# Optimization experiments

Hardware: AMD Instinct MI355X
Metric: run time of the kernel (lower is better)

Reference implementation:

```python
import jax, jax.numpy as jnp
import numpy as np

BN_EPS = 1e-5
LRELU_SLOPE = 0.2


def setup_inputs() -> dict:
    key = jax.random.key(0)
    ks = jax.random.split(key, 5)
    B, C1, M, C2, N, C_out = 8, 256, 4096, 128, 16384, 256
    feature = jax.random.normal(ks[0], (B, C1, M), dtype=jnp.float32)
    encoder_feature = jax.random.normal(ks[1], (B, C2, N), dtype=jnp.float32)
    interp_index = jax.random.randint(ks[2], (B, N, 1), 0, M, dtype=jnp.int64)
    # ConvTranspose1d(384, 256, 1) weight has shape [in, out, 1] -> store as [in, out]
    W = jax.random.normal(ks[3], (C1 + C2, C_out), dtype=jnp.float32) * 0.05
    b = jax.random.normal(ks[4], (C_out,), dtype=jnp.float32) * 0.05
    gamma = jnp.ones((C_out,), dtype=jnp.float32)
    beta = jnp.zeros((C_out,), dtype=jnp.float32)
    return {"feature": feature, "encoder_feature": encoder_feature,
            "interp_index": interp_index, "W": W, "b": b,
            "gamma": gamma, "beta": beta}


def reference(feature, encoder_feature, interp_index, W, b, gamma, beta):
    # feature: [B, C1, M], encoder_feature: [B, C2, N], interp_index: [B, N, 1]
    idx = interp_index[..., 0]                                  # [B, N]
    # index_points on feature.permute(0,2,1) then permute back == gather along last dim
    interp_feature = jnp.take_along_axis(feature, idx[:, None, :], axis=2)  # [B, C1, N]
    x = jnp.concatenate([encoder_feature, interp_feature], axis=1)          # [B, C1+C2, N]
    # ConvTranspose1d(kernel=1): y[b,o,n] = sum_i x[b,i,n] * W[i,o] + b[o]
    y = jnp.einsum('bin,io->bon', x, W) + b[None, :, None]      # [B, C_out, N]
    # BatchNorm1d (training mode: batch stats over (B, N), biased variance)
    mean = jnp.mean(y, axis=(0, 2), keepdims=True)
    var = jnp.mean(jnp.square(y - mean), axis=(0, 2), keepdims=True)
    y = (y - mean) * jax.lax.rsqrt(var + BN_EPS)
    y = y * gamma[None, :, None] + beta[None, :, None]
    # LeakyReLU(0.2)
    return jnp.where(y > 0, y, LRELU_SLOPE * y)
```

## Files before the change

### kernel.cpp

```cpp
#include <hip/hip_runtime.h>
#include <hip/hip_bf16.h>

#define C1    256
#define C2    128
#define COUT  256
#define MM    4096
#define NN    16384
#define BB    8
#define BN_EPS 1e-5f
#define SLOPE 0.2f

typedef float  f32x4  __attribute__((ext_vector_type(4)));
typedef __bf16 bf16x8 __attribute__((ext_vector_type(8)));
typedef unsigned short u16x8 __attribute__((ext_vector_type(8)));

#define GLOBAL_AS __attribute__((address_space(1)))
#define LDS_AS    __attribute__((address_space(3)))

static __device__ __forceinline__ unsigned short f2bf(float f) {
    unsigned int u = __builtin_bit_cast(unsigned int, f);
    unsigned int r = (u + 0x7FFFu + ((u >> 16) & 1u)) >> 16;
    return (unsigned short)r;
}

static __device__ __forceinline__ bf16x8 ld_frag(const unsigned short* p) {
    union { u16x8 s; bf16x8 b; } cvt;
    cvt.s = *reinterpret_cast<const u16x8*>(p);
    return cvt.b;
}

__global__ __launch_bounds__(256, 4) void k1_zt(const float* __restrict__ feature,
                                                const float* __restrict__ W,
                                                float* __restrict__ Zt) {
    const int mt = blockIdx.x;
    const int ot = blockIdx.y;
    const int b  = blockIdx.z;
    const int mb = mt * 64, ob = ot * 64;
    const int tid = threadIdx.x;

    __shared__ unsigned short sA[64 * 136];
    __shared__ unsigned short sB[64 * 136];

    const int wid = tid >> 6, lane = tid & 63;
    const int r = lane & 15, g = lane >> 4;
    const int wm = (wid >> 1) * 32, wo = (wid & 1) * 32;

    f32x4 acc[2][2];
#pragma unroll
    for (int i = 0; i < 2; i++)
#pragma unroll
        for (int j = 0; j < 2; j++) acc[i][j] = (f32x4){0.f, 0.f, 0.f, 0.f};

    for (int kp = 0; kp < 2; kp++) {
        const int k0 = kp * 128;
        for (int p = tid; p < 64 * 16; p += 256) {
            int m = p & 63, k = (p >> 6) << 3;
            u16x8 u;
#pragma unroll
            for (int j = 0; j < 8; j++)
                u[j] = f2bf(feature[(size_t)(b * C1 + k0 + k + j) * MM + mb + m]);
            *reinterpret_cast<u16x8*>(&sA[m * 136 + k]) = u;
        }
        for (int p = tid; p < 64 * 16; p += 256) {
            int o = p & 63, k = (p >> 6) << 3;
            u16x8 u;
#pragma unroll
            for (int j = 0; j < 8; j++)
                u[j] = f2bf(W[(C2 + k0 + k + j) * COUT + ob + o]);
            *reinterpret_cast<u16x8*>(&sB[o * 136 + k]) = u;
        }
        __syncthreads();

#pragma unroll
        for (int ks = 0; ks < 4; ks++) {
            const int kb = ks * 32 + g * 8;
            bf16x8 a0 = ld_frag(&sA[(wm +  0 + r) * 136 + kb]);
            bf16x8 a1 = ld_frag(&sA[(wm + 16 + r) * 136 + kb]);
            bf16x8 b0 = ld_frag(&sB[(wo +  0 + r) * 136 + kb]);
            bf16x8 b1 = ld_frag(&sB[(wo + 16 + r) * 136 + kb]);
            acc[0][0] = __builtin_amdgcn_mfma_f32_16x16x32_bf16(a0, b0, acc[0][0], 0, 0, 0);
            acc[0][1] = __builtin_amdgcn_mfma_f32_16x16x32_bf16(a0, b1, acc[0][1], 0, 0, 0);
            acc[1][0] = __builtin_amdgcn_mfma_f32_16x16x32_bf16(a1, b0, acc[1][0], 0, 0, 0);
            acc[1][1] = __builtin_amdgcn_mfma_f32_16x16x32_bf16(a1, b1, acc[1][1], 0, 0, 0);
        }
        __syncthreads();
    }

#pragma unroll
    for (int fm = 0; fm < 2; fm++)
#pragma unroll
        for (int fo = 0; fo < 2; fo++)
#pragma unroll
            for (int i = 0; i < 4; i++) {
                int m = mb + wm + fm * 16 + g * 4 + i;
                int o = ob + wo + fo * 16 + r;
                Zt[((size_t)b * MM + m) * COUT + o] = acc[fm][fo][i];
            }
}

__global__ __launch_bounds__(256, 4) void k2_main(const float* __restrict__ enc,
                                                  const float* __restrict__ W,
                                                  const float* __restrict__ bias,
                                                  const int*   __restrict__ idx,
                                                  const float* __restrict__ Zt,
                                                  float* __restrict__ y,
                                                  float* __restrict__ sums,
                                                  float* __restrict__ sumsq) {
    const int nt = blockIdx.x;
    const int ot = blockIdx.y;
    const int b  = blockIdx.z;
    const int nb = nt * 128, ob = ot * 64;
    const int tid = threadIdx.x;

    __shared__ unsigned short sB[128 * 136];
    __shared__ float lsum[64], lsq[64];

    if (tid < 64) { lsum[tid] = 0.f; lsq[tid] = 0.f; }

    const int wid = tid >> 6, lane = tid & 63;
    const int r = lane & 15, g = lane >> 4;
    const int wo = (wid >> 1) * 32;
    const int wn = (wid & 1) * 64;

    bf16x8 wf[4][2];
#pragma unroll
    for (int ks = 0; ks < 4; ks++)
#pragma unroll
        for (int fr = 0; fr < 2; fr++) {
            u16x8 tmp;
#pragma unroll
            for (int j = 0; j < 8; j++)
                tmp[j] = f2bf(W[(ks * 32 + g * 8 + j) * COUT + ob + wo + fr * 16 + r]);
            union { u16x8 u; bf16x8 b; } cv; cv.u = tmp;
            wf[ks][fr] = cv.b;
        }

    for (int p = tid; p < 128 * 16; p += 256) {
        int n = p & 127, k = (p >> 7) << 3;
        u16x8 u;
#pragma unroll
        for (int j = 0; j < 8; j++)
            u[j] = f2bf(enc[(size_t)(b * C2 + k + j) * NN + nb + n]);
        *reinterpret_cast<u16x8*>(&sB[n * 136 + k]) = u;
    }
    __syncthreads();

    f32x4 acc[2][4];
#pragma unroll
    for (int i = 0; i < 2; i++)
#pragma unroll
        for (int j = 0; j < 4; j++) acc[i][j] = (f32x4){0.f, 0.f, 0.f, 0.f};

#pragma unroll
    for (int ks = 0; ks < 4; ks++) {
        const int kb = ks * 32 + g * 8;
        bf16x8 bfr[4];
#pragma unroll
        for (int fn = 0; fn < 4; fn++)
            bfr[fn] = ld_frag(&sB[(wn + fn * 16 + r) * 136 + kb]);
#pragma unroll
        for (int fn = 0; fn < 4; fn++) {
            acc[0][fn] = __builtin_amdgcn_mfma_f32_16x16x32_bf16(wf[ks][0], bfr[fn], acc[0][fn], 0, 0, 0);
            acc[1][fn] = __builtin_amdgcn_mfma_f32_16x16x32_bf16(wf[ks][1], bfr[fn], acc[1][fn], 0, 0, 0);
        }
    }
    __syncthreads();

    float* Zl = reinterpret_cast<float*>(sB);
    {
        const int lrow = lane >> 4;
        const int lcol = lane & 15;
        const int* idxb = idx + b * NN + nb;
#pragma unroll
        for (int it = 0; it < 8; it++) {
            const int wrow = wid * 32 + it * 4;
            const int row  = wrow + lrow;
            const int zi   = idxb[row];
            const float* src = &Zt[((size_t)b * MM + zi) * COUT + ob +
                                   ((lcol ^ (row & 15)) << 2)];
            __builtin_amdgcn_global_load_lds(
                (const GLOBAL_AS unsigned int*)src,
                (LDS_AS unsigned int*)(&Zl[wrow * 64]), 16, 0, 0);
        }
    }
    __syncthreads();

    float bi[2][4];
#pragma unroll
    for (int fo = 0; fo < 2; fo++)
#pragma unroll
        for (int i = 0; i < 4; i++)
            bi[fo][i] = bias[ob + wo + fo * 16 + g * 4 + i];

    float s_[2][4] = {{0.f,0.f,0.f,0.f},{0.f,0.f,0.f,0.f}};
    float q_[2][4] = {{0.f,0.f,0.f,0.f},{0.f,0.f,0.f,0.f}};
#pragma unroll
    for (int fo = 0; fo < 2; fo++)
#pragma unroll
        for (int fn = 0; fn < 4; fn++) {
            const int n_loc = wn + fn * 16 + r;
            const int o4 = (wo >> 2) + fo * 4 + g;
            const f32x4 z = *reinterpret_cast<const f32x4*>(
                &Zl[n_loc * 64 + ((o4 ^ r) << 2)]);
#pragma unroll
            for (int i = 0; i < 4; i++) {
                int o_loc = wo + fo * 16 + g * 4 + i;
                float v = acc[fo][fn][i] + z[i] + bi[fo][i];
                y[(size_t)(b * COUT + ob + o_loc) * NN + nb + n_loc] = v;
                s_[fo][i] += v;
                q_[fo][i] += v * v;
            }
        }

#pragma unroll
    for (int d = 1; d < 16; d <<= 1)
#pragma unroll
        for (int fo = 0; fo < 2; fo++)
#pragma unroll
            for (int i = 0; i < 4; i++) {
                s_[fo][i] += __shfl_xor(s_[fo][i], d);
                q_[fo][i] += __shfl_xor(q_[fo][i], d);
            }
    if (r == 0) {
#pragma unroll
        for (int fo = 0; fo < 2; fo++)
#pragma unroll
            for (int i = 0; i < 4; i++) {
                int o_loc = wo + fo * 16 + g * 4 + i;
                atomicAdd(&lsum[o_loc], s_[fo][i]);
                atomicAdd(&lsq[o_loc],  q_[fo][i]);
            }
    }
    __syncthreads();
    if (tid < 64) {
        atomicAdd(&sums [b * COUT + ob + tid], lsum[tid]);
        atomicAdd(&sumsq[b * COUT + ob + tid], lsq[tid]);
    }
}

__global__ void k3_stats(const float* __restrict__ sums,
                         const float* __restrict__ sumsq,
                         const float* __restrict__ gamma,
                         const float* __restrict__ beta,
                         float* __restrict__ ac) {
    const int o = threadIdx.x;
    float s = 0.f, q = 0.f;
#pragma unroll
    for (int b = 0; b < BB; b++) {
        s += sums [b * COUT + o];
        q += sumsq[b * COUT + o];
    }
    const float inv_cnt = 1.0f / ((float)BB * (float)NN);
    float mean = s * inv_cnt;
    float var  = q * inv_cnt - mean * mean;
    float a = gamma[o] * rsqrtf(var + BN_EPS);
    float c = beta[o] - mean * a;
    ac[o] = a;
    ac[COUT + o] = c;
}

__global__ __launch_bounds__(256) void k4_norm(float* __restrict__ y,
                                               const float* __restrict__ ac) {
    const size_t total4 = (size_t)BB * COUT * NN / 4;
    const size_t stride = (size_t)gridDim.x * 256;
    for (size_t i = (size_t)blockIdx.x * 256 + threadIdx.x; i < total4; i += stride) {
        float4 v = reinterpret_cast<float4*>(y)[i];
        int o = (int)((i * 4) >> 14) & 255;
        float a = ac[o], c = ac[COUT + o];
        float t0 = a * v.x + c; v.x = t0 > 0.f ? t0 : SLOPE * t0;
        float t1 = a * v.y + c; v.y = t1 > 0.f ? t1 : SLOPE * t1;
        float t2 = a * v.z + c; v.z = t2 > 0.f ? t2 : SLOPE * t2;
        float t3 = a * v.w + c; v.w = t3 > 0.f ? t3 : SLOPE * t3;
        reinterpret_cast<float4*>(y)[i] = v;
    }
}

extern "C" void kernel_launch(void* const* d_in, const int* in_sizes, int n_in,
                              void* d_out, int out_size, void* d_ws, size_t ws_size,
                              hipStream_t stream) {
    const float* feature = (const float*)d_in[0];
    const float* enc     = (const float*)d_in[1];
    const int*   idx     = (const int*)  d_in[2];
    const float* W       = (const float*)d_in[3];
    const float* bias    = (const float*)d_in[4];
    const float* gamma   = (const float*)d_in[5];
    const float* beta    = (const float*)d_in[6];
    float* out = (float*)d_out;

    float* sums  = (float*)d_ws;
    float* sumsq = sums + BB * COUT;
    float* ac    = sumsq + BB * COUT;
    float* Zt    = ac + 2 * COUT;

    hipMemsetAsync(sums, 0, 2 * BB * COUT * sizeof(float), stream);

    k1_zt  <<<dim3(MM / 64, COUT / 64, BB), 256, 0, stream>>>(feature, W, Zt);
    k2_main<<<dim3(NN / 128, COUT / 64, BB), 256, 0, stream>>>(enc, W, bias, idx, Zt,
                                                               out, sums, sumsq);
    k3_stats<<<1, COUT, 0, stream>>>(sums, sumsq, gamma, beta, ac);
    k4_norm<<<2048, 256, 0, stream>>>(out, ac);
}
```

Measured before the change: 325.3 us.

## Pre-transpose inputs to bf16 and store gathered Z table in bf16

Adds a transpose kernel that converts feature, encoder_feature and W into K-contiguous bf16 copies, so the GEMM kernels read MFMA fragments straight from global memory instead of doing strided fp32 loads and converting into LDS. The intermediate Z table is now stored in bf16, which halves the bytes written by k1 and read by the gather in k2. The gather is issued before the encoder GEMM so it can overlap with it. The cost is three extra launches plus an extra pass that reads and writes the inputs, and Z loses some precision.

```diff
diff --git a/kernel.cpp b/kernel.cpp
--- a/kernel.cpp
+++ b/kernel.cpp
@@ -4,6 +4,7 @@
 #define C1    256
 #define C2    128
 #define COUT  256
+#define KTOT  384
 #define MM    4096
 #define NN    16384
 #define BB    8
@@ -13,6 +14,7 @@
 typedef float  f32x4  __attribute__((ext_vector_type(4)));
 typedef __bf16 bf16x8 __attribute__((ext_vector_type(8)));
 typedef unsigned short u16x8 __attribute__((ext_vector_type(8)));
+typedef unsigned short u16x4 __attribute__((ext_vector_type(4)));
 
 #define GLOBAL_AS __attribute__((address_space(1)))
 #define LDS_AS    __attribute__((address_space(3)))
@@ -23,24 +25,48 @@
     return (unsigned short)r;
 }
 
-static __device__ __forceinline__ bf16x8 ld_frag(const unsigned short* p) {
+static __device__ __forceinline__ float bf2f(unsigned short b) {
+    return __builtin_bit_cast(float, (unsigned int)b << 16);
+}
+
+static __device__ __forceinline__ bf16x8 ld_frag_g(const unsigned short* p) {
     union { u16x8 s; bf16x8 b; } cvt;
     cvt.s = *reinterpret_cast<const u16x8*>(p);
     return cvt.b;
 }
 
-__global__ __launch_bounds__(256, 4) void k1_zt(const float* __restrict__ feature,
-                                                const float* __restrict__ W,
-                                                float* __restrict__ Zt) {
-    const int mt = blockIdx.x;
-    const int ot = blockIdx.y;
-    const int b  = blockIdx.z;
-    const int mb = mt * 64, ob = ot * 64;
+__global__ __launch_bounds__(256) void k0_transpose(const float* __restrict__ in,
+                                                    unsigned short* __restrict__ out,
+                                                    int R, int C) {
+    __shared__ float f[64][68];
+    const int c0 = blockIdx.x * 64, r0 = blockIdx.y * 64;
+    const float* inb = in + (size_t)blockIdx.z * R * C;
+    unsigned short* outb = out + (size_t)blockIdx.z * R * C;
+    const int t = threadIdx.x;
+#pragma unroll
+    for (int q = 0; q < 4; q++) {
+        int idx = q * 256 + t;
+        int ri = idx >> 4, c4 = (idx & 15) * 4;
+        float4 v = *reinterpret_cast<const float4*>(&inb[(size_t)(r0 + ri) * C + c0 + c4]);
+        *reinterpret_cast<float4*>(&f[ri][c4]) = v;
+    }
+    __syncthreads();
+#pragma unroll
+    for (int q = 0; q < 4; q++) {
+        int idx = q * 256 + t;
+        int oc = idx >> 4, rq = (idx & 15) * 4;
+        u16x4 u;
+#pragma unroll
+        for (int j = 0; j < 4; j++) u[j] = f2bf(f[rq + j][oc]);
+        *reinterpret_cast<u16x4*>(&outb[(size_t)(c0 + oc) * R + r0 + rq]) = u;
+    }
+}
+
+__global__ __launch_bounds__(256, 4) void k1_zt(const unsigned short* __restrict__ featT,
+                                                const unsigned short* __restrict__ Wt,
+                                                unsigned short* __restrict__ ZtB) {
+    const int mb = blockIdx.x * 64, ob = blockIdx.y * 64, b = blockIdx.z;
     const int tid = threadIdx.x;
-
-    __shared__ unsigned short sA[64 * 136];
-    __shared__ unsigned short sB[64 * 136];
-
     const int wid = tid >> 6, lane = tid & 63;
     const int r = lane & 15, g = lane >> 4;
     const int wm = (wid >> 1) * 32, wo = (wid & 1) * 32;
@@ -51,40 +77,22 @@
 #pragma unroll
         for (int j = 0; j < 2; j++) acc[i][j] = (f32x4){0.f, 0.f, 0.f, 0.f};
 
-    for (int kp = 0; kp < 2; kp++) {
-        const int k0 = kp * 128;
-        for (int p = tid; p < 64 * 16; p += 256) {
-            int m = p & 63, k = (p >> 6) << 3;
-            u16x8 u;
-#pragma unroll
-            for (int j = 0; j < 8; j++)
-                u[j] = f2bf(feature[(size_t)(b * C1 + k0 + k + j) * MM + mb + m]);
-            *reinterpret_cast<u16x8*>(&sA[m * 136 + k]) = u;
-        }
-        for (int p = tid; p < 64 * 16; p += 256) {
-            int o = p & 63, k = (p >> 6) << 3;
-            u16x8 u;
-#pragma unroll
-            for (int j = 0; j < 8; j++)
-                u[j] = f2bf(W[(C2 + k0 + k + j) * COUT + ob + o]);
-            *reinterpret_cast<u16x8*>(&sB[o * 136 + k]) = u;
-        }
-        __syncthreads();
-
+    const unsigned short* fA = featT + (size_t)(b * MM + mb) * C1;
+
+#pragma unroll
+    for (int kp = 0; kp < 2; kp++)
 #pragma unroll
         for (int ks = 0; ks < 4; ks++) {
-            const int kb = ks * 32 + g * 8;
-            bf16x8 a0 = ld_frag(&sA[(wm +  0 + r) * 136 + kb]);
-            bf16x8 a1 = ld_frag(&sA[(wm + 16 + r) * 136 + kb]);
-            bf16x8 b0 = ld_frag(&sB[(wo +  0 + r) * 136 + kb]);
-            bf16x8 b1 = ld_frag(&sB[(wo + 16 + r) * 136 + kb]);
+            const int kb = kp * 128 + ks * 32 + g * 8;
+            bf16x8 a0 = ld_frag_g(&fA[(size_t)(wm +  0 + r) * C1 + kb]);
+            bf16x8 a1 = ld_frag_g(&fA[(size_t)(wm + 16 + r) * C1 + kb]);
+            bf16x8 b0 = ld_frag_g(&Wt[(size_t)(ob + wo +  0 + r) * KTOT + C2 + kb]);
+            bf16x8 b1 = ld_frag_g(&Wt[(size_t)(ob + wo + 16 + r) * KTOT + C2 + kb]);
             acc[0][0] = __builtin_amdgcn_mfma_f32_16x16x32_bf16(a0, b0, acc[0][0], 0, 0, 0);
             acc[0][1] = __builtin_amdgcn_mfma_f32_16x16x32_bf16(a0, b1, acc[0][1], 0, 0, 0);
             acc[1][0] = __builtin_amdgcn_mfma_f32_16x16x32_bf16(a1, b0, acc[1][0], 0, 0, 0);
             acc[1][1] = __builtin_amdgcn_mfma_f32_16x16x32_bf16(a1, b1, acc[1][1], 0, 0, 0);
         }
-        __syncthreads();
-    }
 
 #pragma unroll
     for (int fm = 0; fm < 2; fm++)
@@ -94,27 +102,23 @@
             for (int i = 0; i < 4; i++) {
                 int m = mb + wm + fm * 16 + g * 4 + i;
                 int o = ob + wo + fo * 16 + r;
-                Zt[((size_t)b * MM + m) * COUT + o] = acc[fm][fo][i];
-            }
-}
-
-__global__ __launch_bounds__(256, 4) void k2_main(const float* __restrict__ enc,
-                                                  const float* __restrict__ W,
+                ZtB[(size_t)(b * MM + m) * COUT + o] = f2bf(acc[fm][fo][i]);
+            }
+}
+
+__global__ __launch_bounds__(256, 4) void k2_main(const unsigned short* __restrict__ encT,
+                                                  const unsigned short* __restrict__ Wt,
                                                   const float* __restrict__ bias,
                                                   const int*   __restrict__ idx,
-                                                  const float* __restrict__ Zt,
+                                                  const unsigned short* __restrict__ ZtB,
                                                   float* __restrict__ y,
                                                   float* __restrict__ sums,
                                                   float* __restrict__ sumsq) {
-    const int nt = blockIdx.x;
-    const int ot = blockIdx.y;
-    const int b  = blockIdx.z;
-    const int nb = nt * 128, ob = ot * 64;
+    const int nb = blockIdx.x * 128, ob = blockIdx.y * 64, b = blockIdx.z;
     const int tid = threadIdx.x;
 
-    __shared__ unsigned short sB[128 * 136];
+    __shared__ unsigned short ZlB[128 * 64];
     __shared__ float lsum[64], lsq[64];
-
     if (tid < 64) { lsum[tid] = 0.f; lsq[tid] = 0.f; }
 
     const int wid = tid >> 6, lane = tid & 63;
@@ -122,28 +126,29 @@
     const int wo = (wid >> 1) * 32;
     const int wn = (wid & 1) * 64;
 
+    {
+        const int* idxb = idx + b * NN + nb;
+        const int lrow = lane >> 3, lcol = lane & 7;
+#pragma unroll
+        for (int it = 0; it < 4; it++) {
+            const int wrow = wid * 32 + it * 8;
+            const int row  = wrow + lrow;
+            const int zi   = idxb[row];
+            const unsigned short* src = &ZtB[(size_t)(b * MM + zi) * COUT + ob +
+                                             ((lcol ^ (row & 7)) << 3)];
+            __builtin_amdgcn_global_load_lds(
+                (const GLOBAL_AS unsigned int*)src,
+                (LDS_AS unsigned int*)(&ZlB[wrow * 64]), 16, 0, 0);
+        }
+    }
+
     bf16x8 wf[4][2];
 #pragma unroll
     for (int ks = 0; ks < 4; ks++)
 #pragma unroll
-        for (int fr = 0; fr < 2; fr++) {
-            u16x8 tmp;
-#pragma unroll
-            for (int j = 0; j < 8; j++)
-                tmp[j] = f2bf(W[(ks * 32 + g * 8 + j) * COUT + ob + wo + fr * 16 + r]);
-            union { u16x8 u; bf16x8 b; } cv; cv.u = tmp;
-            wf[ks][fr] = cv.b;
-        }
-
-    for (int p = tid; p < 128 * 16; p += 256) {
-        int n = p & 127, k = (p >> 7) << 3;
-        u16x8 u;
-#pragma unroll
-        for (int j = 0; j < 8; j++)
-            u[j] = f2bf(enc[(size_t)(b * C2 + k + j) * NN + nb + n]);
-        *reinterpret_cast<u16x8*>(&sB[n * 136 + k]) = u;
-    }
-    __syncthreads();
+        for (int fr = 0; fr < 2; fr++)
+            wf[ks][fr] = ld_frag_g(&Wt[(size_t)(ob + wo + fr * 16 + r) * KTOT +
+                                       ks * 32 + g * 8]);
 
     f32x4 acc[2][4];
 #pragma unroll
@@ -151,38 +156,21 @@
 #pragma unroll
         for (int j = 0; j < 4; j++) acc[i][j] = (f32x4){0.f, 0.f, 0.f, 0.f};
 
+    const unsigned short* eB = encT + (size_t)(b * NN + nb) * C2;
 #pragma unroll
     for (int ks = 0; ks < 4; ks++) {
         const int kb = ks * 32 + g * 8;
         bf16x8 bfr[4];
 #pragma unroll
         for (int fn = 0; fn < 4; fn++)
-            bfr[fn] = ld_frag(&sB[(wn + fn * 16 + r) * 136 + kb]);
+            bfr[fn] = ld_frag_g(&eB[(size_t)(wn + fn * 16 + r) * C2 + kb]);
 #pragma unroll
         for (int fn = 0; fn < 4; fn++) {
             acc[0][fn] = __builtin_amdgcn_mfma_f32_16x16x32_bf16(wf[ks][0], bfr[fn], acc[0][fn], 0, 0, 0);
             acc[1][fn] = __builtin_amdgcn_mfma_f32_16x16x32_bf16(wf[ks][1], bfr[fn], acc[1][fn], 0, 0, 0);
         }
     }
-    __syncthreads();
-
-    float* Zl = reinterpret_cast<float*>(sB);
-    {
-        const int lrow = lane >> 4;
-        const int lcol = lane & 15;
-        const int* idxb = idx + b * NN + nb;
-#pragma unroll
-        for (int it = 0; it < 8; it++) {
-            const int wrow = wid * 32 + it * 4;
-            const int row  = wrow + lrow;
-            const int zi   = idxb[row];
-            const float* src = &Zt[((size_t)b * MM + zi) * COUT + ob +
-                                   ((lcol ^ (row & 15)) << 2)];
-            __builtin_amdgcn_global_load_lds(
-                (const GLOBAL_AS unsigned int*)src,
-                (LDS_AS unsigned int*)(&Zl[wrow * 64]), 16, 0, 0);
-        }
-    }
+
     __syncthreads();
 
     float bi[2][4];
@@ -199,13 +187,15 @@
 #pragma unroll
         for (int fn = 0; fn < 4; fn++) {
             const int n_loc = wn + fn * 16 + r;
-            const int o4 = (wo >> 2) + fo * 4 + g;
-            const f32x4 z = *reinterpret_cast<const f32x4*>(
-                &Zl[n_loc * 64 + ((o4 ^ r) << 2)]);
-#pragma unroll
-            for (int i = 0; i < 4; i++) {
-                int o_loc = wo + fo * 16 + g * 4 + i;
-                float v = acc[fo][fn][i] + z[i] + bi[fo][i];
+            const int obase = wo + fo * 16 + g * 4;
+            const int pg = (obase >> 3) ^ (n_loc & 7);
+            const int h  = (obase >> 2) & 1;
+            const u16x4 z = *reinterpret_cast<const u16x4*>(
+                &ZlB[n_loc * 64 + (pg << 3) + (h << 2)]);
+#pragma unroll
+            for (int i = 0; i < 4; i++) {
+                int o_loc = obase + i;
+                float v = acc[fo][fn][i] + bf2f(z[i]) + bi[fo][i];
                 y[(size_t)(b * COUT + ob + o_loc) * NN + nb + n_loc] = v;
                 s_[fo][i] += v;
                 q_[fo][i] += v * v;
@@ -290,12 +280,19 @@
     float* sums  = (float*)d_ws;
     float* sumsq = sums + BB * COUT;
     float* ac    = sumsq + BB * COUT;
-    float* Zt    = ac + 2 * COUT;
+    unsigned short* ZtB   = (unsigned short*)(ac + 2 * COUT);
+    unsigned short* featT = ZtB   + (size_t)BB * MM * COUT;
+    unsigned short* encT  = featT + (size_t)BB * MM * C1;
+    unsigned short* Wt    = encT  + (size_t)BB * NN * C2;
 
     hipMemsetAsync(sums, 0, 2 * BB * COUT * sizeof(float), stream);
 
-    k1_zt  <<<dim3(MM / 64, COUT / 64, BB), 256, 0, stream>>>(feature, W, Zt);
-    k2_main<<<dim3(NN / 128, COUT / 64, BB), 256, 0, stream>>>(enc, W, bias, idx, Zt,
+    k0_transpose<<<dim3(MM / 64, C1 / 64, BB),   256, 0, stream>>>(feature, featT, C1, MM);
+    k0_transpose<<<dim3(NN / 64, C2 / 64, BB),   256, 0, stream>>>(enc, encT, C2, NN);
+    k0_transpose<<<dim3(COUT / 64, KTOT / 64, 1),256, 0, stream>>>(W, Wt, KTOT, COUT);
+
+    k1_zt  <<<dim3(MM / 64, COUT / 64, BB), 256, 0, stream>>>(featT, Wt, ZtB);
+    k2_main<<<dim3(NN / 128, COUT / 64, BB), 256, 0, stream>>>(encT, Wt, bias, idx, ZtB,
                                                                out, sums, sumsq);
     k3_stats<<<1, COUT, 0, stream>>>(sums, sumsq, gamma, beta, ac);
     k4_norm<<<2048, 256, 0, stream>>>(out, ac);
```

Result: slower. 346.9 us (+6.6%).
